# Optimization experiments

Measured on AMD Instinct MI355X. Metric: run time of the kernel, lower is better.

Reference implementation:

```python
import jax, jax.numpy as jnp
import numpy as np
from math import factorial

L_MAX = 3
RC = 5.0
N_BASIS = 8
N_MAX = 4
N_CH = 16
K = N_MAX * N_CH  # 64 combined (radial x element-channel) features per l
NU_SCALING = 1.0
MP_SCALING = 0.5
OVERALL_SCALING = 1.0


def _fact(n):
    return float(factorial(n))


def _clebsch(j1, m1, j2, m2, J, M):
    # Racah formula for complex-basis Clebsch-Gordan coefficients
    if m1 + m2 != M or J < abs(j1 - j2) or J > j1 + j2:
        return 0.0
    pref = ((2 * J + 1) * _fact(J + j1 - j2) * _fact(J - j1 + j2) * _fact(j1 + j2 - J) / _fact(j1 + j2 + J + 1)) ** 0.5
    pref *= (_fact(J + M) * _fact(J - M) * _fact(j1 - m1) * _fact(j1 + m1) * _fact(j2 - m2) * _fact(j2 + m2)) ** 0.5
    s = 0.0
    for k in range(0, j1 + j2 - J + 1):
        d = [k, j1 + j2 - J - k, j1 - m1 - k, j2 + m2 - k, J - j2 + m1 + k, J - j1 - m2 + k]
        if min(d) < 0:
            continue
        den = 1.0
        for v in d:
            den *= _fact(v)
        s += (-1) ** k / den
    return pref * s


def _u_real(l):
    # complex -> real spherical-harmonic change of basis
    U = np.zeros((2 * l + 1, 2 * l + 1), dtype=complex)
    U[l, l] = 1.0
    for m in range(1, l + 1):
        U[l + m, l + m] = (-1) ** m / np.sqrt(2)
        U[l + m, l - m] = 1.0 / np.sqrt(2)
        U[l - m, l - m] = 1j / np.sqrt(2)
        U[l - m, l + m] = -1j * (-1) ** m / np.sqrt(2)
    return U


def _real_cg(l1, l2, L):
    Cc = np.zeros((2 * l1 + 1, 2 * l2 + 1, 2 * L + 1), dtype=complex)
    for m1 in range(-l1, l1 + 1):
        for m2 in range(-l2, l2 + 1):
            M = m1 + m2
            if abs(M) <= L:
                Cc[l1 + m1, l2 + m2, L + M] = _clebsch(l1, m1, l2, m2, L, M)
    T = np.einsum('am,bn,co,mno->abc', _u_real(l1), _u_real(l2), _u_real(L).conj(), Cc)
    re, im = T.real, T.imag
    out = re if np.abs(re).sum() >= np.abs(im).sum() else im
    return out.astype(np.float32)


CG = {}
for _l1 in range(L_MAX + 1):
    for _l2 in range(L_MAX + 1):
        for _L in range(abs(_l1 - _l2), min(_l1 + _l2, L_MAX) + 1):
            CG[(_l1, _l2, _L)] = jnp.asarray(_real_cg(_l1, _l2, _L))


def _spherical_harmonics(u):
    # real spherical harmonics up to l=3 on unit vectors, list of [E, 2l+1]
    x, y, z = u[:, 0], u[:, 1], u[:, 2]
    Y0 = 0.28209479177387814 * jnp.ones_like(x)[:, None]
    c1 = 0.4886025119029199
    Y1 = jnp.stack([c1 * y, c1 * z, c1 * x], axis=1)
    Y2 = jnp.stack([
        1.0925484305920792 * x * y,
        1.0925484305920792 * y * z,
        0.31539156525252005 * (3.0 * z * z - 1.0),
        1.0925484305920792 * x * z,
        0.5462742152960396 * (x * x - y * y),
    ], axis=1)
    Y3 = jnp.stack([
        0.5900435899266435 * y * (3.0 * x * x - y * y),
        2.890611442640554 * x * y * z,
        0.4570457994644658 * y * (5.0 * z * z - 1.0),
        0.3731763325901154 * z * (5.0 * z * z - 3.0),
        0.4570457994644658 * x * (5.0 * z * z - 1.0),
        1.445305721320277 * z * (x * x - y * y),
        0.5900435899266435 * x * (x * x - 3.0 * y * y),
    ], axis=1)
    return [Y0, Y1, Y2, Y3]


def _forward(positions, embeddings, W_inv, W_eq, W_mlp1, W_mlp2, w_last, species, senders, receivers):
    n_atoms = positions.shape[0]
    rij = positions[receivers] - positions[senders]            # [E,3]
    d = jnp.sqrt(jnp.sum(rij * rij, axis=1) + 1e-12)           # [E]
    u = rij / d[:, None]
    sh = [NU_SCALING * Y for Y in _spherical_harmonics(u)]
    fc = 0.5 * (jnp.cos(jnp.pi * d / RC) + 1.0) * (d < RC)     # smooth cutoff
    mu = jnp.asarray(np.linspace(0.0, RC, N_BASIS).astype(np.float32))
    sigma = RC / N_BASIS
    basis = jnp.exp(-0.5 * ((d[:, None] - mu) / sigma) ** 2) * fc[:, None]  # [E,B]
    emb = embeddings[species]                  # [N,C] center element embeddings
    emb_k = jnp.tile(emb, (1, N_MAX))          # [N,K]
    x_nb = emb[senders]                        # [E,C]
    # --- invariant message passing -> spherical expansion, list of [N, 2l+1, K]
    feats = []
    for l in range(L_MAX + 1):
        R = basis @ W_inv[l]                   # [E, N_MAX]
        msg = jnp.einsum('em,en,ec->emnc', sh[l], R, x_nb).reshape(-1, 2 * l + 1, K)
        feats.append(MP_SCALING * jax.ops.segment_sum(msg, receivers, num_segments=n_atoms))
    # --- generalized CG self-iteration (nu_max = 2 -> one iteration), residual
    new = []
    for L in range(L_MAX + 1):
        acc = feats[L]
        for l1 in range(L_MAX + 1):
            for l2 in range(L_MAX + 1):
                if (l1, l2, L) in CG:
                    acc = acc + jnp.einsum('nik,njk,ijm->nmk', feats[l1], feats[l2], CG[(l1, l2, L)])
        new.append(acc)
    feats = new
    # --- equivariant message passing layer (n_mp_layers = 2 -> one layer)
    embedded = [f * emb_k[:, None, :] for f in feats]
    nb = [f[senders] for f in embedded]        # gather sender features per l
    mp = []
    for L in range(L_MAX + 1):
        R = basis @ W_eq[L]                    # [E,K] learned radial weights
        acc = jnp.zeros((n_atoms, 2 * L + 1, K), dtype=positions.dtype)
        for l1 in range(L_MAX + 1):
            for l2 in range(L_MAX + 1):
                if (l1, l2, L) in CG:
                    m = jnp.einsum('ea,ebk,abM->eMk', sh[l1], nb[l2], CG[(l1, l2, L)])
                    acc = acc + jax.ops.segment_sum(m * R[:, None, :], receivers, num_segments=n_atoms)
        mp.append(MP_SCALING * acc)
    # --- final CG iterator requesting only L=0 invariants ('0_1')
    inv = mp[0][:, 0, :]
    for l in range(L_MAX + 1):
        inv = inv + jnp.einsum('nik,njk,ij->nk', mp[l], mp[l], CG[(l, l, 0)][:, :, 0])
    # --- invariant MLP + last layer, sum over atoms
    h = jax.nn.silu(inv @ W_mlp1)
    h = jax.nn.silu(h @ W_mlp2)
    e_atom = h @ w_last
    return (OVERALL_SCALING * jnp.sum(e_atom)).reshape(1)


def setup_inputs():
    key = jax.random.key(0)
    ks = jax.random.split(key, 10)
    N, E, NSPEC = 10000, 160000, 4
    return {
        'positions': jax.random.uniform(ks[0], (N, 3), dtype=jnp.float32) * 10.0,
        'embeddings': jax.random.normal(ks[4], (NSPEC, N_CH), dtype=jnp.float32),
        'W_inv': jax.random.normal(ks[5], (L_MAX + 1, N_BASIS, N_MAX), dtype=jnp.float32) / np.float32(np.sqrt(N_BASIS)),
        'W_eq': jax.random.normal(ks[6], (L_MAX + 1, N_BASIS, K), dtype=jnp.float32) / np.float32(np.sqrt(N_BASIS)),
        'W_mlp1': jax.random.normal(ks[7], (K, K), dtype=jnp.float32) / np.float32(np.sqrt(K)),
        'W_mlp2': jax.random.normal(ks[8], (K, K), dtype=jnp.float32) / np.float32(np.sqrt(K)),
        'w_last': jax.random.normal(ks[9], (K,), dtype=jnp.float32) / np.float32(np.sqrt(K)),
        'species': jax.random.randint(ks[1], (N,), 0, NSPEC),
        'senders': jax.random.randint(ks[2], (E,), 0, N),
        'receivers': jax.random.randint(ks[3], (E,), 0, N),
    }


def reference(positions, embeddings, W_inv, W_eq, W_mlp1, W_mlp2, w_last, species, senders, receivers):
    return _forward(positions, embeddings, W_inv, W_eq, W_mlp1, W_mlp2, w_last, species, senders, receivers)
```

## Files before the change

kernel.cpp:

```cpp
#include <hip/hip_runtime.h>
#include <math.h>

#define L_MAX 3
#define RCUT 5.0f
#define NB 8
#define NCH 16
#define KDIM 64
#define LMDIM 16
#define GSTRIDE 40


struct CD { double re; double im; };
struct UMat { CD m[7][7]; };
struct CGT { float v[7][7][7]; };

constexpr double cfact(int n){ double r=1.0; for(int i=2;i<=n;++i) r*=(double)i; return r; }
constexpr double cfabs(double x){ return x<0.0 ? -x : x; }
constexpr double csqrt_(double x){
  if (x<=0.0) return 0.0;
  double g = x>1.0 ? x : 1.0;
  for (int i=0;i<100;++i) g = 0.5*(g + x/g);
  return g;
}
constexpr double clebsch(int j1,int m1,int j2,int m2,int J,int M){
  if (m1+m2!=M) return 0.0;
  int ad = j1-j2; if (ad<0) ad=-ad;
  if (J<ad || J>j1+j2) return 0.0;
  double pref = csqrt_((2.0*J+1.0)*cfact(J+j1-j2)*cfact(J-j1+j2)*cfact(j1+j2-J)/cfact(j1+j2+J+1));
  pref *= csqrt_(cfact(J+M)*cfact(J-M)*cfact(j1-m1)*cfact(j1+m1)*cfact(j2-m2)*cfact(j2+m2));
  double s=0.0;
  for (int k=0;k<=j1+j2-J;++k){
    int d0=k,d1=j1+j2-J-k,d2=j1-m1-k,d3=j2+m2-k,d4=J-j2+m1+k,d5=J-j1-m2+k;
    if (d0<0||d1<0||d2<0||d3<0||d4<0||d5<0) continue;
    double den = cfact(d0)*cfact(d1)*cfact(d2)*cfact(d3)*cfact(d4)*cfact(d5);
    s += ((k&1)? -1.0:1.0)/den;
  }
  return pref*s;
}
constexpr UMat u_real(int l){
  UMat U{};
  U.m[l][l] = CD{1.0, 0.0};
  double is2 = csqrt_(0.5);
  for (int mm=1; mm<=l; ++mm){
    double sgn = (mm&1)? -1.0: 1.0;
    U.m[l+mm][l+mm] = CD{sgn*is2, 0.0};
    U.m[l+mm][l-mm] = CD{is2, 0.0};
    U.m[l-mm][l-mm] = CD{0.0, is2};
    U.m[l-mm][l+mm] = CD{0.0, -sgn*is2};
  }
  return U;
}
constexpr CGT real_cg(int l1,int l2,int L){
  double Cc[7][7][7] = {};
  for (int m1=-l1;m1<=l1;++m1)
    for (int m2=-l2;m2<=l2;++m2){
      int M=m1+m2;
      if (M>=-L && M<=L) Cc[l1+m1][l2+m2][L+M] = clebsch(l1,m1,l2,m2,L,M);
    }
  UMat U1=u_real(l1), U2=u_real(l2), U3=u_real(L);
  double Tre[7][7][7]={}, Tim[7][7][7]={};
  for (int a=0;a<2*l1+1;++a)
   for (int m=0;m<2*l1+1;++m){
     CD u1=U1.m[a][m];
     if (u1.re==0.0 && u1.im==0.0) continue;
     for (int b=0;b<2*l2+1;++b)
      for (int n=0;n<2*l2+1;++n){
        CD u2=U2.m[b][n];
        if (u2.re==0.0 && u2.im==0.0) continue;
        CD u12 = CD{u1.re*u2.re-u1.im*u2.im, u1.re*u2.im+u1.im*u2.re};
        for (int c=0;c<2*L+1;++c)
         for (int o=0;o<2*L+1;++o){
           CD u3=U3.m[c][o];
           if (u3.re==0.0 && u3.im==0.0) continue;
           double cc=Cc[m][n][o];
           if (cc==0.0) continue;
           double tr = u12.re*u3.re + u12.im*u3.im;
           double ti = u12.im*u3.re - u12.re*u3.im;
           Tre[a][b][c] += tr*cc;
           Tim[a][b][c] += ti*cc;
         }
      }
   }
  double sre=0.0, sim=0.0;
  for (int a=0;a<2*l1+1;++a) for (int b=0;b<2*l2+1;++b) for (int c=0;c<2*L+1;++c){
    sre += cfabs(Tre[a][b][c]); sim += cfabs(Tim[a][b][c]);
  }
  CGT out{};
  bool ure = (sre>=sim);
  for (int a=0;a<2*l1+1;++a) for (int b=0;b<2*l2+1;++b) for (int c=0;c<2*L+1;++c)
    out.v[a][b][c] = (float)(ure? Tre[a][b][c] : Tim[a][b][c]);
  return out;
}

struct alignas(64) CFlat { float v[256][16]; };
constexpr CFlat build_cflat(){
  CFlat o{};
  for (int l1=0;l1<=3;++l1)
   for (int l2=0;l2<=3;++l2){
     int lo = l1>l2 ? l1-l2 : l2-l1;
     int hi = (l1+l2<3)? l1+l2 : 3;
     for (int L=lo; L<=hi; ++L){
       CGT cg = real_cg(l1,l2,L);
       for (int i=0;i<2*l1+1;++i)
        for (int j=0;j<2*l2+1;++j)
         for (int m=0;m<2*L+1;++m){
           o.v[(L*L+m)*16 + (l2*l2+j)][l1*l1+i] += 0.5f*cg.v[i][j][m];
         }
     }
   }
  return o;
}
__device__ const CFlat CFLAT = build_cflat();

struct CSym { float v[16][16][16]; };
constexpr CSym build_csym(){
  CSym o{};
  for (int l1=0;l1<=3;++l1)
   for (int l2=0;l2<=3;++l2){
     int lo = l1>l2 ? l1-l2 : l2-l1;
     int hi = (l1+l2<3)? l1+l2 : 3;
     for (int L=lo; L<=hi; ++L){
       CGT cg = real_cg(l1,l2,L);
       for (int i=0;i<2*l1+1;++i)
        for (int j=0;j<2*l2+1;++j)
         for (int m=0;m<2*L+1;++m)
           o.v[L*L+m][l1*l1+i][l2*l2+j] += cg.v[i][j][m];
     }
   }
  for (int M=0;M<16;++M)
   for (int i=0;i<16;++i)
    for (int j=i+1;j<16;++j){
      o.v[M][i][j] += o.v[M][j][i];
      o.v[M][j][i] = 0.0f;
    }
  return o;
}

template<int M>
__device__ __forceinline__ float tp_row(const float* __restrict__ f){
  constexpr CSym CS = build_csym();
  float g = 0.0f;
  #pragma unroll
  for (int i=0;i<16;++i)
  #pragma unroll
  for (int j=i;j<16;++j){
    float c = CS.v[M][i][j];
    if (c != 0.0f) g += c * f[i] * f[j];
  }
  return g;
}

template<int l>
__device__ __forceinline__ float inv_term(const float* m){
  constexpr CGT cg = real_cg(l,l,0);
  float a=0.0f;
  #pragma unroll
  for (int i=0;i<2*l+1;++i)
  #pragma unroll
  for (int j=0;j<2*l+1;++j){
    float c = cg.v[i][j][0];
    if (c != 0.0f) a += c*m[l*l+i]*m[l*l+j];
  }
  return a;
}

__device__ __forceinline__ void compute_sh(float x, float y, float z, float* sh){
  sh[0]  = 0.28209479177387814f;
  sh[1]  = 0.4886025119029199f*y;
  sh[2]  = 0.4886025119029199f*z;
  sh[3]  = 0.4886025119029199f*x;
  sh[4]  = 1.0925484305920792f*x*y;
  sh[5]  = 1.0925484305920792f*y*z;
  sh[6]  = 0.31539156525252005f*(3.0f*z*z-1.0f);
  sh[7]  = 1.0925484305920792f*x*z;
  sh[8]  = 0.5462742152960396f*(x*x-y*y);
  sh[9]  = 0.5900435899266435f*y*(3.0f*x*x-y*y);
  sh[10] = 2.890611442640554f*x*y*z;
  sh[11] = 0.4570457994644658f*y*(5.0f*z*z-1.0f);
  sh[12] = 0.3731763325901154f*z*(5.0f*z*z-3.0f);
  sh[13] = 0.4570457994644658f*x*(5.0f*z*z-1.0f);
  sh[14] = 1.445305721320277f*z*(x*x-y*y);
  sh[15] = 0.5900435899266435f*x*(x*x-3.0f*y*y);
}

__global__ __launch_bounds__(256) void k_hist_d(
    const float* __restrict__ pos, const int* __restrict__ senders,
    const int* __restrict__ recv, int* __restrict__ counts, int E)
{
  int e = blockIdx.x*256 + threadIdx.x;
  if (e >= E) return;
  int s = senders[e], r = recv[e];
  float dx = pos[r*3+0]-pos[s*3+0];
  float dy = pos[r*3+1]-pos[s*3+1];
  float dz = pos[r*3+2]-pos[s*3+2];
  float d  = sqrtf(dx*dx+dy*dy+dz*dz + 1e-12f);
  if (d < RCUT) atomicAdd(&counts[r], 1);
}

__global__ __launch_bounds__(256) void k_scan1(const int* __restrict__ counts,
                                               int* __restrict__ offsets,
                                               int* __restrict__ bsum, int N){
  __shared__ int buf[256];
  int i = blockIdx.x*256 + threadIdx.x;
  int v = (i<N)? counts[i] : 0;
  buf[threadIdx.x] = v;
  __syncthreads();
  #pragma unroll
  for (int o=1;o<256;o<<=1){
    int t = (threadIdx.x>=o)? buf[threadIdx.x-o] : 0;
    __syncthreads();
    buf[threadIdx.x] += t;
    __syncthreads();
  }
  if (i<N) offsets[i] = buf[threadIdx.x] - v;
  if (threadIdx.x==255) bsum[blockIdx.x] = buf[255];
}

__global__ __launch_bounds__(256) void k_scan2(const int* __restrict__ bsum,
                                               int* __restrict__ bbase, int SB){
  __shared__ int buf[256];
  int v = (threadIdx.x<SB)? bsum[threadIdx.x] : 0;
  buf[threadIdx.x] = v;
  __syncthreads();
  #pragma unroll
  for (int o=1;o<256;o<<=1){
    int t = (threadIdx.x>=o)? buf[threadIdx.x-o] : 0;
    __syncthreads();
    buf[threadIdx.x] += t;
    __syncthreads();
  }
  if (threadIdx.x<SB) bbase[threadIdx.x] = buf[threadIdx.x] - v;
}

__global__ __launch_bounds__(256) void k_scan3(int* __restrict__ offsets,
                                               const int* __restrict__ bbase, int N){
  int i = blockIdx.x*256 + threadIdx.x;
  if (i<N) offsets[i] += bbase[blockIdx.x];
}

__global__ __launch_bounds__(256) void k_geom(
    const float* __restrict__ pos, const float* __restrict__ Winv,
    const int* __restrict__ species,
    const int* __restrict__ senders, const int* __restrict__ recv,
    const int* __restrict__ offsets, int* __restrict__ cursor,
    int* __restrict__ bucket_s, float* __restrict__ geomArr, int E)
{
  int e = blockIdx.x*256 + threadIdx.x;
  if (e >= E) return;
  int s = senders[e], r = recv[e];
  float dx = pos[r*3+0]-pos[s*3+0];
  float dy = pos[r*3+1]-pos[s*3+1];
  float dz = pos[r*3+2]-pos[s*3+2];
  float d  = sqrtf(dx*dx+dy*dy+dz*dz + 1e-12f);
  if (d >= RCUT) return;
  int p = atomicAdd(&cursor[r], 1);
  int slot = offsets[r] + p;
  float inv_d = 1.0f/d;
  float sh[16];
  compute_sh(dx*inv_d, dy*inv_d, dz*inv_d, sh);
  float fc = 0.5f*(cosf(d*(3.14159265358979323846f/RCUT))+1.0f);
  float b[8];
  #pragma unroll
  for (int q=0;q<NB;++q){
    float t = (d - (float)((double)q*(5.0/7.0))) * 1.6f;
    b[q] = expf(-0.5f*t*t)*fc;
  }
  float* g = geomArr + (size_t)slot*GSTRIDE;
  #pragma unroll
  for (int i=0;i<16;++i) g[i] = sh[i];
  #pragma unroll
  for (int q=0;q<8;++q) g[16+q] = b[q];
  #pragma unroll
  for (int l=0;l<4;++l)
    #pragma unroll
    for (int n=0;n<4;++n){
      float acc=0.0f;
      #pragma unroll
      for (int q=0;q<NB;++q) acc += b[q]*Winv[l*32+q*4+n];
      g[24+l*4+n] = acc;
    }
  bucket_s[slot] = s | (species[s]<<16);
}

__global__ __launch_bounds__(64) void kA_gather_tp(
    const float* __restrict__ emb, const int* __restrict__ species,
    const int* __restrict__ offsets, const int* __restrict__ counts,
    const int* __restrict__ bucket_s, const float* __restrict__ geomArr,
    float* __restrict__ feats, int N)
{
  int r = blockIdx.x;
  if (r >= N) return;
  int lane = threadIdx.x;
  int n = lane>>4, c = lane&15;
  int off = offsets[r], cnt = counts[r];
  float f[16];
  #pragma unroll
  for (int lm=0; lm<16; ++lm) f[lm]=0.0f;

  float e5_c = 0.0f;
  float4 s0c{},s1c{},s2c{},s3c{};
  float R0c=0,R1c=0,R2c=0,R3c=0;
  if (cnt>0){
    int pk = bucket_s[off];
    e5_c = 0.5f*emb[(pk>>16)*NCH+c];
    const float* gm = geomArr + (size_t)off*GSTRIDE;
    s0c=*(const float4*)(gm+0); s1c=*(const float4*)(gm+4);
    s2c=*(const float4*)(gm+8); s3c=*(const float4*)(gm+12);
    R0c=gm[24+0+n]; R1c=gm[24+4+n]; R2c=gm[24+8+n]; R3c=gm[24+12+n];
  }
  for (int j=0; j<cnt; ++j){
    bool hn = (j+1<cnt);
    int pk_n = hn ? bucket_s[off+j+1] : 0;
    float e5_n = hn ? 0.5f*emb[(pk_n>>16)*NCH+c] : 0.0f;
    const float* gn = geomArr + (size_t)(off+(hn?j+1:j))*GSTRIDE;
    float4 s0n=*(const float4*)(gn+0), s1n=*(const float4*)(gn+4);
    float4 s2n=*(const float4*)(gn+8), s3n=*(const float4*)(gn+12);
    float R0n=gn[24+0+n], R1n=gn[24+4+n], R2n=gn[24+8+n], R3n=gn[24+12+n];

    float t0 = R0c*e5_c, t1 = R1c*e5_c, t2 = R2c*e5_c, t3 = R3c*e5_c;
    f[0] += s0c.x*t0;
    f[1] += s0c.y*t1;  f[2] += s0c.z*t1;  f[3] += s0c.w*t1;
    f[4] += s1c.x*t2;  f[5] += s1c.y*t2;  f[6] += s1c.z*t2;  f[7] += s1c.w*t2;  f[8] += s2c.x*t2;
    f[9] += s2c.y*t3;  f[10]+= s2c.z*t3;  f[11]+= s2c.w*t3;
    f[12]+= s3c.x*t3;  f[13]+= s3c.y*t3;  f[14]+= s3c.z*t3;  f[15]+= s3c.w*t3;

    e5_c=e5_n; s0c=s0n; s1c=s1n; s2c=s2n; s3c=s3n;
    R0c=R0n; R1c=R1n; R2c=R2n; R3c=R3n;
  }
  float g[16];
  g[0]=tp_row<0>(f);  g[1]=tp_row<1>(f);  g[2]=tp_row<2>(f);  g[3]=tp_row<3>(f);
  g[4]=tp_row<4>(f);  g[5]=tp_row<5>(f);  g[6]=tp_row<6>(f);  g[7]=tp_row<7>(f);
  g[8]=tp_row<8>(f);  g[9]=tp_row<9>(f);  g[10]=tp_row<10>(f); g[11]=tp_row<11>(f);
  g[12]=tp_row<12>(f); g[13]=tp_row<13>(f); g[14]=tp_row<14>(f); g[15]=tp_row<15>(f);
  float ek = emb[species[r]*NCH + c];
  float* fp = feats + (size_t)r*(LMDIM*KDIM) + lane*LMDIM;
  float4* fp4 = (float4*)fp;
  fp4[0] = make_float4((f[0]+g[0])*ek,  (f[1]+g[1])*ek,  (f[2]+g[2])*ek,  (f[3]+g[3])*ek);
  fp4[1] = make_float4((f[4]+g[4])*ek,  (f[5]+g[5])*ek,  (f[6]+g[6])*ek,  (f[7]+g[7])*ek);
  fp4[2] = make_float4((f[8]+g[8])*ek,  (f[9]+g[9])*ek,  (f[10]+g[10])*ek,(f[11]+g[11])*ek);
  fp4[3] = make_float4((f[12]+g[12])*ek,(f[13]+g[13])*ek,(f[14]+g[14])*ek,(f[15]+g[15])*ek);
}

__global__ __launch_bounds__(64) void kB_mp2_mlp(
    const float* __restrict__ Weq,
    const float* __restrict__ W1, const float* __restrict__ W2,
    const float* __restrict__ wl,
    const int* __restrict__ offsets, const int* __restrict__ counts,
    const int* __restrict__ bucket_s, const float* __restrict__ geomArr,
    const float* __restrict__ embedded, float* __restrict__ eatom, int N)
{
  __shared__ __align__(16) float Arow[256];
  int r = blockIdx.x;
  if (r >= N) return;
  int k = threadIdx.x;
  int off = offsets[r], cnt = counts[r];
  float Wq[4][8];
  #pragma unroll
  for (int L=0;L<4;++L)
    #pragma unroll
    for (int q=0;q<8;++q)
      Wq[L][q] = Weq[L*(NB*KDIM) + q*KDIM + k];
  float m[16];
  #pragma unroll
  for (int i=0;i<16;++i) m[i]=0.0f;

  float4 nb0c{}, nb1c{}, nb2c{}, nb3c{};
  {
    int pk0 = (cnt>0)? bucket_s[off] : 0;
    const float4* np0 = (const float4*)(embedded + (size_t)(pk0 & 0xFFFF)*(LMDIM*KDIM) + k*LMDIM);
    if (cnt>0){ nb0c=np0[0]; nb1c=np0[1]; nb2c=np0[2]; nb3c=np0[3]; }
  }
  for (int j=0; j<cnt; ++j){
    bool hn = (j+1<cnt);
    int pk_n = hn ? bucket_s[off+j+1] : 0;
    const float4* npn = (const float4*)(embedded + (size_t)(pk_n & 0xFFFF)*(LMDIM*KDIM) + k*LMDIM);
    float4 nb0n{}, nb1n{}, nb2n{}, nb3n{};
    if (hn){ nb0n=npn[0]; nb1n=npn[1]; nb2n=npn[2]; nb3n=npn[3]; }

    const float* gm = geomArr + (size_t)(off+j)*GSTRIDE;
    float4 s0 = *(const float4*)(gm+0);
    float4 s1 = *(const float4*)(gm+4);
    float4 s2 = *(const float4*)(gm+8);
    float4 s3 = *(const float4*)(gm+12);
    float4 b0 = *(const float4*)(gm+16);
    float4 b1 = *(const float4*)(gm+20);
    float sh[16] = {s0.x,s0.y,s0.z,s0.w, s1.x,s1.y,s1.z,s1.w,
                    s2.x,s2.y,s2.z,s2.w, s3.x,s3.y,s3.z,s3.w};
    float b[8] = {b0.x,b0.y,b0.z,b0.w, b1.x,b1.y,b1.z,b1.w};
    float Req[4];
    #pragma unroll
    for (int L=0;L<4;++L){
      float acc=0.0f;
      #pragma unroll
      for (int q=0;q<8;++q) acc += b[q]*Wq[L][q];
      Req[L]=acc;
    }
    #pragma unroll
    for (int q=0;q<4;++q){
      int ent = q*64 + k;
      const float4* c4 = (const float4*)CFLAT.v[ent];
      float4 c0=c4[0], c1=c4[1], c2=c4[2], c3=c4[3];
      float acc = c0.x*sh[0]+c0.y*sh[1]+c0.z*sh[2]+c0.w*sh[3]
                + c1.x*sh[4]+c1.y*sh[5]+c1.z*sh[6]+c1.w*sh[7]
                + c2.x*sh[8]+c2.y*sh[9]+c2.z*sh[10]+c2.w*sh[11]
                + c3.x*sh[12]+c3.y*sh[13]+c3.z*sh[14]+c3.w*sh[15];
      Arow[ent] = acc;
    }
    float nb_c[16] = {nb0c.x,nb0c.y,nb0c.z,nb0c.w, nb1c.x,nb1c.y,nb1c.z,nb1c.w,
                      nb2c.x,nb2c.y,nb2c.z,nb2c.w, nb3c.x,nb3c.y,nb3c.z,nb3c.w};
    #pragma unroll
    for (int M=0;M<16;++M){
      const int L = (M==0)?0 : (M<4)?1 : (M<9)?2 : 3;
      const float4* a4 = (const float4*)(Arow + M*16);
      float4 a0=a4[0], a1=a4[1], a2=a4[2], a3=a4[3];
      float acc = a0.x*nb_c[0]+a0.y*nb_c[1]+a0.z*nb_c[2]+a0.w*nb_c[3]
                + a1.x*nb_c[4]+a1.y*nb_c[5]+a1.z*nb_c[6]+a1.w*nb_c[7]
                + a2.x*nb_c[8]+a2.y*nb_c[9]+a2.z*nb_c[10]+a2.w*nb_c[11]
                + a3.x*nb_c[12]+a3.y*nb_c[13]+a3.z*nb_c[14]+a3.w*nb_c[15];
      m[M] += acc*Req[L];
    }
    nb0c=nb0n; nb1c=nb1n; nb2c=nb2n; nb3c=nb3n;
  }

  float inv = m[0];
  inv += inv_term<0>(m);
  inv += inv_term<1>(m);
  inv += inv_term<2>(m);
  inv += inv_term<3>(m);
  Arow[k] = inv;
  float a=0.0f;
  #pragma unroll
  for (int c=0;c<64;++c) a += Arow[c]*W1[c*64+k];
  a = a / (1.0f + expf(-a));
  Arow[64+k] = a;
  float h2=0.0f;
  #pragma unroll
  for (int c=0;c<64;++c) h2 += Arow[64+c]*W2[c*64+k];
  h2 = h2 / (1.0f + expf(-h2));
  float e = h2*wl[k];
  #pragma unroll
  for (int o=32; o>0; o>>=1) e += __shfl_down(e, o);
  if (k==0) eatom[r] = e;
}

__global__ __launch_bounds__(256) void k_reduce(const float* __restrict__ eatom,
                                                float* __restrict__ out, int N){
  __shared__ float buf[256];
  float a=0.0f;
  for (int i=threadIdx.x; i<N; i+=256) a += eatom[i];
  buf[threadIdx.x]=a;
  __syncthreads();
  #pragma unroll
  for (int o=128;o>0;o>>=1){
    if (threadIdx.x<o) buf[threadIdx.x]+=buf[threadIdx.x+o];
    __syncthreads();
  }
  if (threadIdx.x==0) out[0]=buf[0];
}

extern "C" void kernel_launch(void* const* d_in, const int* in_sizes, int n_in,
                              void* d_out, int out_size, void* d_ws, size_t ws_size,
                              hipStream_t stream)
{
  const float* pos     = (const float*)d_in[0];
  const float* emb     = (const float*)d_in[1];
  const float* Winv    = (const float*)d_in[2];
  const float* Weq     = (const float*)d_in[3];
  const float* W1      = (const float*)d_in[4];
  const float* W2      = (const float*)d_in[5];
  const float* wl      = (const float*)d_in[6];
  const int*   species = (const int*)d_in[7];
  const int*   senders = (const int*)d_in[8];
  const int*   recv    = (const int*)d_in[9];
  int N = in_sizes[7];
  int E = in_sizes[8];

  char* ws = (char*)d_ws;
  float* feats   = (float*)ws;
  float* geomArr = feats + (size_t)N*(LMDIM*KDIM);
  float* eatom   = geomArr + (size_t)E*GSTRIDE;
  int*   counts  = (int*)(eatom + N);
  int*   cursor  = counts + N;
  int*   offsets = cursor + N;
  int*   bsum    = offsets + N;
  int*   bbase   = bsum + 256;
  int*   bucket_s= bbase + 256;

  hipMemsetAsync(counts, 0, 2*(size_t)N*sizeof(int), stream);

  int ebl = (E+255)/256;
  int SB  = (N+255)/256;
  k_hist_d<<<ebl, 256, 0, stream>>>(pos, senders, recv, counts, E);
  k_scan1<<<SB, 256, 0, stream>>>(counts, offsets, bsum, N);
  k_scan2<<<1, 256, 0, stream>>>(bsum, bbase, SB);
  k_scan3<<<SB, 256, 0, stream>>>(offsets, bbase, N);
  k_geom<<<ebl, 256, 0, stream>>>(pos, Winv, species, senders, recv, offsets, cursor,
                                  bucket_s, geomArr, E);
  kA_gather_tp<<<N, 64, 0, stream>>>(emb, species, offsets, counts, bucket_s, geomArr, feats, N);
  kB_mp2_mlp<<<N, 64, 0, stream>>>(Weq, W1, W2, wl, offsets, counts, bucket_s, geomArr,
                                   feats, eatom, N);
  k_reduce<<<1, 256, 0, stream>>>(eatom, (float*)d_out, N);
}
```

Before: 231.1 us.

## Accumulate per-receiver species-binned SH×radial sums with atomics, expand per node

Each in-cutoff edge now adds sh·R into a per-receiver table indexed by the sender's species (4×16×4 floats) using float atomics inside the geometry kernel. The per-node gather loop over bucketed edges is replaced by a small expansion kernel that contracts the table with the 4 species embeddings. This removes the serial per-edge gather and the 64-lane redundant reads, but adds 64 global atomics per edge, a larger memset, and order-dependent float summation.

```diff
diff --git a/kernel.cpp b/kernel.cpp
--- a/kernel.cpp
+++ b/kernel.cpp
@@ -243,7 +243,8 @@
     const int* __restrict__ species,
     const int* __restrict__ senders, const int* __restrict__ recv,
     const int* __restrict__ offsets, int* __restrict__ cursor,
-    int* __restrict__ bucket_s, float* __restrict__ geomArr, int E)
+    int* __restrict__ bucket_s, float* __restrict__ geomArr,
+    float* __restrict__ T, int E)
 {
   int e = blockIdx.x*256 + threadIdx.x;
   if (e >= E) return;
@@ -265,6 +266,7 @@
     float t = (d - (float)((double)q*(5.0/7.0))) * 1.6f;
     b[q] = expf(-0.5f*t*t)*fc;
   }
+  float R[4][4];
   float* g = geomArr + (size_t)slot*GSTRIDE;
   #pragma unroll
   for (int i=0;i<16;++i) g[i] = sh[i];
@@ -277,55 +279,40 @@
       float acc=0.0f;
       #pragma unroll
       for (int q=0;q<NB;++q) acc += b[q]*Winv[l*32+q*4+n];
+      R[l][n]=acc;
       g[24+l*4+n] = acc;
     }
-  bucket_s[slot] = s | (species[s]<<16);
-}
-
-__global__ __launch_bounds__(64) void kA_gather_tp(
+  int spec = species[s];
+  bucket_s[slot] = s | (spec<<16);
+  float* Tr = T + (size_t)r*256 + spec*64;
+  #pragma unroll
+  for (int lm=0; lm<16; ++lm){
+    const int l = (lm==0)?0 : (lm<4)?1 : (lm<9)?2 : 3;
+    #pragma unroll
+    for (int n=0;n<4;++n)
+      atomicAdd(&Tr[lm*4+n], sh[lm]*R[l][n]);
+  }
+}
+
+__global__ __launch_bounds__(256) void kA_expand(
     const float* __restrict__ emb, const int* __restrict__ species,
-    const int* __restrict__ offsets, const int* __restrict__ counts,
-    const int* __restrict__ bucket_s, const float* __restrict__ geomArr,
-    float* __restrict__ feats, int N)
+    const float* __restrict__ T, float* __restrict__ feats, int N)
 {
-  int r = blockIdx.x;
+  __shared__ float Ts[4][256];
+  int wv = threadIdx.x>>6, lane = threadIdx.x & 63;
+  int r = blockIdx.x*4 + wv;
   if (r >= N) return;
-  int lane = threadIdx.x;
   int n = lane>>4, c = lane&15;
-  int off = offsets[r], cnt = counts[r];
+  const float4* T4 = (const float4*)(T + (size_t)r*256);
+  ((float4*)Ts[wv])[lane] = T4[lane];
   float f[16];
   #pragma unroll
-  for (int lm=0; lm<16; ++lm) f[lm]=0.0f;
-
-  float e5_c = 0.0f;
-  float4 s0c{},s1c{},s2c{},s3c{};
-  float R0c=0,R1c=0,R2c=0,R3c=0;
-  if (cnt>0){
-    int pk = bucket_s[off];
-    e5_c = 0.5f*emb[(pk>>16)*NCH+c];
-    const float* gm = geomArr + (size_t)off*GSTRIDE;
-    s0c=*(const float4*)(gm+0); s1c=*(const float4*)(gm+4);
-    s2c=*(const float4*)(gm+8); s3c=*(const float4*)(gm+12);
-    R0c=gm[24+0+n]; R1c=gm[24+4+n]; R2c=gm[24+8+n]; R3c=gm[24+12+n];
-  }
-  for (int j=0; j<cnt; ++j){
-    bool hn = (j+1<cnt);
-    int pk_n = hn ? bucket_s[off+j+1] : 0;
-    float e5_n = hn ? 0.5f*emb[(pk_n>>16)*NCH+c] : 0.0f;
-    const float* gn = geomArr + (size_t)(off+(hn?j+1:j))*GSTRIDE;
-    float4 s0n=*(const float4*)(gn+0), s1n=*(const float4*)(gn+4);
-    float4 s2n=*(const float4*)(gn+8), s3n=*(const float4*)(gn+12);
-    float R0n=gn[24+0+n], R1n=gn[24+4+n], R2n=gn[24+8+n], R3n=gn[24+12+n];
-
-    float t0 = R0c*e5_c, t1 = R1c*e5_c, t2 = R2c*e5_c, t3 = R3c*e5_c;
-    f[0] += s0c.x*t0;
-    f[1] += s0c.y*t1;  f[2] += s0c.z*t1;  f[3] += s0c.w*t1;
-    f[4] += s1c.x*t2;  f[5] += s1c.y*t2;  f[6] += s1c.z*t2;  f[7] += s1c.w*t2;  f[8] += s2c.x*t2;
-    f[9] += s2c.y*t3;  f[10]+= s2c.z*t3;  f[11]+= s2c.w*t3;
-    f[12]+= s3c.x*t3;  f[13]+= s3c.y*t3;  f[14]+= s3c.z*t3;  f[15]+= s3c.w*t3;
-
-    e5_c=e5_n; s0c=s0n; s1c=s1n; s2c=s2n; s3c=s3n;
-    R0c=R0n; R1c=R1n; R2c=R2n; R3c=R3n;
+  for (int lm=0; lm<16; ++lm){
+    float acc = emb[0*NCH+c]*Ts[wv][0*64+lm*4+n]
+              + emb[1*NCH+c]*Ts[wv][1*64+lm*4+n]
+              + emb[2*NCH+c]*Ts[wv][2*64+lm*4+n]
+              + emb[3*NCH+c]*Ts[wv][3*64+lm*4+n];
+    f[lm] = 0.5f*acc;
   }
   float g[16];
   g[0]=tp_row<0>(f);  g[1]=tp_row<1>(f);  g[2]=tp_row<2>(f);  g[3]=tp_row<3>(f);
@@ -481,12 +468,13 @@
   float* eatom   = geomArr + (size_t)E*GSTRIDE;
   int*   counts  = (int*)(eatom + N);
   int*   cursor  = counts + N;
-  int*   offsets = cursor + N;
+  float* T       = (float*)(cursor + N);
+  int*   offsets = (int*)(T + (size_t)N*256);
   int*   bsum    = offsets + N;
   int*   bbase   = bsum + 256;
   int*   bucket_s= bbase + 256;
 
-  hipMemsetAsync(counts, 0, 2*(size_t)N*sizeof(int), stream);
+  hipMemsetAsync(counts, 0, (size_t)N*(2+256)*sizeof(int), stream);
 
   int ebl = (E+255)/256;
   int SB  = (N+255)/256;
@@ -495,8 +483,8 @@
   k_scan2<<<1, 256, 0, stream>>>(bsum, bbase, SB);
   k_scan3<<<SB, 256, 0, stream>>>(offsets, bbase, N);
   k_geom<<<ebl, 256, 0, stream>>>(pos, Winv, species, senders, recv, offsets, cursor,
-                                  bucket_s, geomArr, E);
-  kA_gather_tp<<<N, 64, 0, stream>>>(emb, species, offsets, counts, bucket_s, geomArr, feats, N);
+                                  bucket_s, geomArr, T, E);
+  kA_expand<<<(N+3)/4, 256, 0, stream>>>(emb, species, T, feats, N);
   kB_mp2_mlp<<<N, 64, 0, stream>>>(Weq, W1, W2, wl, offsets, counts, bucket_s, geomArr,
                                    feats, eatom, N);
   k_reduce<<<1, 256, 0, stream>>>(eatom, (float*)d_out, N);
```

Result: slower. 382.8 us (+65.7%).
